# Performance work log

Hardware: AMD Instinct MI355X
Metric: run time of the kernel (lower is better)

The kernel has to match this reference:

```python
import jax, jax.numpy as jnp
import numpy as np

EMBED = 1024
HEADS = 16
HEAD_DIM = EMBED // HEADS


def setup_inputs() -> dict:
    key = jax.random.key(0)
    ks = jax.random.split(key, 5)
    scale = 1.0 / np.sqrt(EMBED)
    x = jax.random.normal(ks[0], (2, 2048, EMBED), dtype=jnp.float32)
    W_qkv = jax.random.normal(ks[1], (EMBED, 3 * EMBED), dtype=jnp.float32) * scale
    b_qkv = jnp.zeros((3 * EMBED,), dtype=jnp.float32)
    W_out = jax.random.normal(ks[2], (EMBED, EMBED), dtype=jnp.float32) * scale
    b_out = jnp.zeros((EMBED,), dtype=jnp.float32)
    return {"x": x, "W_qkv": W_qkv, "b_qkv": b_qkv, "W_out": W_out, "b_out": b_out}


def reference(x, W_qkv, b_qkv, W_out, b_out):
    B, S, E = x.shape
    # fused QKV projection
    qkv = x @ W_qkv + b_qkv                       # [B, S, 3E]
    qkv = qkv.reshape(B, S, HEADS, 3 * HEAD_DIM)
    q, k, v = jnp.split(qkv, 3, axis=-1)          # each [B, S, H, D]
    scale = jnp.sqrt(jnp.asarray(HEAD_DIM, dtype=x.dtype))
    # scores [B, H, S, S]
    scores = jnp.einsum('bqhd,bkhd->bhqk', q, k) / scale
    attn = jax.nn.softmax(scores, axis=-1)
    out = jnp.einsum('bhqk,bkhd->bqhd', attn, v).reshape(B, S, E)
    return out @ W_out + b_out
```

## Files before the change

kernel.cpp:

```cpp
#include <hip/hip_runtime.h>

#define B_    2
#define S_    2048
#define E_    1024
#define H_    16
#define D_    64
#define M_    4096
#define NQKV  3072
#define K_    1024

typedef __bf16 bf16;
typedef __attribute__((ext_vector_type(4))) __bf16 bf16x4;
typedef __attribute__((ext_vector_type(8))) __bf16 bf16x8;
typedef __attribute__((ext_vector_type(4))) float  f32x4;
typedef __attribute__((ext_vector_type(16))) float f32x16;

#define QSCALE 0.18033688f

__device__ __forceinline__ void gload_lds16(const void* g, void* l) {
    __builtin_amdgcn_global_load_lds(
        (const __attribute__((address_space(1))) void*)g,
        (__attribute__((address_space(3))) void*)l, 16, 0, 0);
}

__global__ __launch_bounds__(256) void cast_f32_bf16(
    const float* __restrict__ in, bf16* __restrict__ out, int n)
{
    int i = (blockIdx.x * 256 + threadIdx.x) * 4;
    if (i >= n) return;
    float4 v = *reinterpret_cast<const float4*>(in + i);
    bf16x4 o = { (bf16)v.x, (bf16)v.y, (bf16)v.z, (bf16)v.w };
    *reinterpret_cast<bf16x4*>(out + i) = o;
}

__global__ __launch_bounds__(256) void transpose_cast(
    const float* __restrict__ W, bf16* __restrict__ WT, int Krows, int Ncols)
{
    __shared__ bf16 tile[32][33];
    int bj = blockIdx.x;
    int bi = blockIdx.y;
    int tx = threadIdx.x & 31;
    int ty = threadIdx.x >> 5;
#pragma unroll
    for (int it = 0; it < 4; ++it) {
        int r = ty + it * 8;
        tile[r][tx] = (bf16)W[(size_t)(bi * 32 + r) * Ncols + bj * 32 + tx];
    }
    __syncthreads();
#pragma unroll
    for (int it = 0; it < 4; ++it) {
        int r = ty + it * 8;
        WT[(size_t)(bj * 32 + r) * Krows + bi * 32 + tx] = tile[tx][r];
    }
}

__device__ __forceinline__ void gemm_tile_128(
    const bf16* __restrict__ A, const bf16* __restrict__ BT, int K,
    int bm0, int bn0, f32x4 acc[4][4])
{
    __shared__ bf16 sA[128 * 32];
    __shared__ bf16 sB[128 * 32];
    const int tid  = threadIdx.x;
    const int lane = tid & 63;
    const int wave = tid >> 6;
    const int g    = lane >> 4;
    const int r    = lane & 15;
    const int wr   = wave >> 1, wc = wave & 1;
    const int lrow = lane >> 2;
    const int lcol = (lane & 3) * 8;

#pragma unroll
    for (int m = 0; m < 4; ++m)
#pragma unroll
        for (int n = 0; n < 4; ++n) acc[m][n] = (f32x4){0.f, 0.f, 0.f, 0.f};

    for (int k0 = 0; k0 < K; k0 += 32) {
#pragma unroll
        for (int j = 0; j < 2; ++j) {
            int r0 = wave * 32 + j * 16;
            gload_lds16(A  + (size_t)(bm0 + r0 + lrow) * K + k0 + lcol, &sA[r0 * 32]);
            gload_lds16(BT + (size_t)(bn0 + r0 + lrow) * K + k0 + lcol, &sB[r0 * 32]);
        }
        __syncthreads();
        bf16x8 af[4], bfr[4];
#pragma unroll
        for (int m = 0; m < 4; ++m)
            af[m] = *reinterpret_cast<const bf16x8*>(&sA[(wr * 64 + m * 16 + r) * 32 + g * 8]);
#pragma unroll
        for (int n = 0; n < 4; ++n)
            bfr[n] = *reinterpret_cast<const bf16x8*>(&sB[(wc * 64 + n * 16 + r) * 32 + g * 8]);
        __builtin_amdgcn_s_setprio(1);
#pragma unroll
        for (int m = 0; m < 4; ++m)
#pragma unroll
            for (int n = 0; n < 4; ++n)
                acc[m][n] = __builtin_amdgcn_mfma_f32_16x16x32_bf16(af[m], bfr[n], acc[m][n], 0, 0, 0);
        __builtin_amdgcn_s_setprio(0);
        __syncthreads();
    }
}

__global__ __launch_bounds__(256) void gemm_qkv(
    const bf16* __restrict__ xb, const bf16* __restrict__ WT,
    const float* __restrict__ bias,
    bf16* __restrict__ Qb, bf16* __restrict__ Kb, bf16* __restrict__ Vt)
{
    f32x4 acc[4][4];
    int bm0 = blockIdx.y * 128, bn0 = blockIdx.x * 128;
    gemm_tile_128(xb, WT, K_, bm0, bn0, acc);

    const int lane = threadIdx.x & 63, wave = threadIdx.x >> 6;
    const int g = lane >> 4, c = lane & 15;
    const int wr = wave >> 1, wc = wave & 1;
#pragma unroll
    for (int m = 0; m < 4; ++m) {
        int ibase = bm0 + wr * 64 + m * 16 + 4 * g;
        int b = ibase >> 11, s = ibase & 2047;
#pragma unroll
        for (int n = 0; n < 4; ++n) {
            int j = bn0 + wc * 64 + n * 16 + c;
            int h = j / 192, w = j % 192;
            int t = w >> 6, d = w & 63;
            float bj = bias[j];
            if (t == 2) {
                bf16x4 v4 = { (bf16)(acc[m][n][0] + bj), (bf16)(acc[m][n][1] + bj),
                              (bf16)(acc[m][n][2] + bj), (bf16)(acc[m][n][3] + bj) };
                *reinterpret_cast<bf16x4*>(
                    &Vt[((size_t)((b * H_ + h) * D_ + d)) * S_ + s]) = v4;
            } else {
                bf16* dst = (t == 0) ? Qb : Kb;
                float scale = (t == 0) ? QSCALE : 1.0f;
#pragma unroll
                for (int jj = 0; jj < 4; ++jj) {
                    size_t idx = ((size_t)((b * H_ + h) * S_ + s + jj)) * D_ + d;
                    dst[idx] = (bf16)((acc[m][n][jj] + bj) * scale);
                }
            }
        }
    }
}

__global__ __launch_bounds__(512, 4) void attn_kernel(
    const bf16* __restrict__ Qb, const bf16* __restrict__ Kb,
    const bf16* __restrict__ Vt, bf16* __restrict__ Ob)
{
    __shared__ __align__(16) char smem[37888];

    const int bh  = blockIdx.y;
    const int q0  = blockIdx.x * 128;
    const int tid = threadIdx.x, lane = tid & 63;
    const int qw   = (tid >> 6) & 3;
    const int half = tid >> 8;
    const int gtid = tid & 255;
    const int c = lane & 31;
    const int h = lane >> 5;

    bf16* sKh = reinterpret_cast<bf16*>(smem) + half * (64 * 72);
    bf16* sVh = reinterpret_cast<bf16*>(smem + 18432) + half * (64 * 72);
    float* mrg = reinterpret_cast<float*>(smem);
    float* ml  = reinterpret_cast<float*>(smem + 36864);

    const bf16* Qp = Qb + (size_t)bh * S_ * D_;
    const bf16* Kp = Kb + (size_t)bh * S_ * D_ + (size_t)half * 1024 * D_;
    const bf16* Vp = Vt + (size_t)bh * D_ * S_ + half * 1024;

    const int qrow = q0 + qw * 32 + c;
    bf16x8 qf[4];
#pragma unroll
    for (int kk = 0; kk < 4; ++kk)
        qf[kk] = *reinterpret_cast<const bf16x8*>(Qp + (size_t)qrow * D_ + kk * 16 + 8 * h);

    f32x16 acc[2];
#pragma unroll
    for (int t = 0; t < 2; ++t) acc[t] = (f32x16)(0.f);
    float m_run = -1e30f, l_run = 0.f;

    const int srow = gtid >> 3, sgi = gtid & 7;

    for (int kv0 = 0; kv0 < 1024; kv0 += 64) {
        __syncthreads();
#pragma unroll
        for (int i = 0; i < 2; ++i) {
            int row = srow + i * 32;
            *reinterpret_cast<uint4*>(&sKh[row * 72 + sgi * 8]) =
                *reinterpret_cast<const uint4*>(Kp + (size_t)(kv0 + row) * D_ + sgi * 8);
            *reinterpret_cast<uint4*>(&sVh[row * 72 + sgi * 8]) =
                *reinterpret_cast<const uint4*>(Vp + (size_t)row * S_ + kv0 + sgi * 8);
        }
        __syncthreads();

#pragma unroll
        for (int ks = 0; ks < 2; ++ks) {
            f32x16 sc = (f32x16)(0.f);
            __builtin_amdgcn_s_setprio(1);
#pragma unroll
            for (int kk = 0; kk < 4; ++kk) {
                bf16x8 kf = *reinterpret_cast<const bf16x8*>(
                    &sKh[(ks * 32 + c) * 72 + kk * 16 + 8 * h]);
                sc = __builtin_amdgcn_mfma_f32_32x32x16_bf16(kf, qf[kk], sc, 0, 0, 0);
            }
            __builtin_amdgcn_s_setprio(0);

            float t0 = fmaxf(fmaxf(sc[0], sc[1]), sc[2]);
            float t1 = fmaxf(fmaxf(sc[3], sc[4]), sc[5]);
            float t2 = fmaxf(fmaxf(sc[6], sc[7]), sc[8]);
            float t3 = fmaxf(fmaxf(sc[9], sc[10]), sc[11]);
            float t4 = fmaxf(fmaxf(sc[12], sc[13]), sc[14]);
            float t5 = fmaxf(fmaxf(t0, t1), sc[15]);
            float t6 = fmaxf(fmaxf(t2, t3), t4);
            float vmax = fmaxf(t5, t6);
            vmax = fmaxf(vmax, __shfl_xor(vmax, 32));
            if (__any(vmax > m_run + 8.0f)) {
                float mnew = fmaxf(m_run, vmax);
                float f = exp2f(m_run - mnew);
                l_run *= f;
#pragma unroll
                for (int t = 0; t < 2; ++t) acc[t] *= f;
                m_run = mnew;
            }
            float p[16];
            float ls = 0.f;
#pragma unroll
            for (int r = 0; r < 16; ++r) { p[r] = exp2f(sc[r] - m_run); ls += p[r]; }
            l_run += ls;

            unsigned w[8];
#pragma unroll
            for (int b = 0; b < 4; ++b) {
                union { bf16 x; unsigned short u; } a0, a1, a2, a3;
                a0.x = (bf16)p[4 * b + 0]; a1.x = (bf16)p[4 * b + 1];
                a2.x = (bf16)p[4 * b + 2]; a3.x = (bf16)p[4 * b + 3];
                w[2 * b]     = (unsigned)a0.u | ((unsigned)a1.u << 16);
                w[2 * b + 1] = (unsigned)a2.u | ((unsigned)a3.u << 16);
            }

#pragma unroll
            for (int kk = 0; kk < 2; ++kk) {
                unsigned s_lo = h ? w[4 * kk]     : w[4 * kk + 2];
                unsigned s_hi = h ? w[4 * kk + 1] : w[4 * kk + 3];
                unsigned r_lo = __shfl_xor(s_lo, 32);
                unsigned r_hi = __shfl_xor(s_hi, 32);
                union { bf16x8 v; unsigned u[4]; } pf;
                if (h == 0) {
                    pf.u[0] = w[4 * kk]; pf.u[1] = w[4 * kk + 1];
                    pf.u[2] = r_lo;      pf.u[3] = r_hi;
                } else {
                    pf.u[0] = r_lo;      pf.u[1] = r_hi;
                    pf.u[2] = w[4 * kk + 2]; pf.u[3] = w[4 * kk + 3];
                }
                __builtin_amdgcn_s_setprio(1);
#pragma unroll
                for (int t = 0; t < 2; ++t) {
                    bf16x8 vf = *reinterpret_cast<const bf16x8*>(
                        &sVh[(32 * t + c) * 72 + ks * 32 + kk * 16 + 8 * h]);
                    acc[t] = __builtin_amdgcn_mfma_f32_32x32x16_bf16(vf, pf.v, acc[t], 0, 0, 0);
                }
                __builtin_amdgcn_s_setprio(0);
            }
        }
    }

    float l_tot = l_run + __shfl_xor(l_run, 32);

    __syncthreads();
    if (half == 1) {
        float4* dst = reinterpret_cast<float4*>(&mrg[(qw * 64 + lane) * 33]);
#pragma unroll
        for (int t = 0; t < 2; ++t)
#pragma unroll
            for (int v = 0; v < 4; ++v)
                dst[t * 4 + v] = make_float4(acc[t][4 * v + 0], acc[t][4 * v + 1],
                                             acc[t][4 * v + 2], acc[t][4 * v + 3]);
        if (lane < 32) { ml[(qw * 32 + lane) * 2 + 0] = m_run;
                         ml[(qw * 32 + lane) * 2 + 1] = l_tot; }
    }
    __syncthreads();

    if (half == 0) {
        float m1 = ml[(qw * 32 + c) * 2 + 0], l1 = ml[(qw * 32 + c) * 2 + 1];
        float mm = fmaxf(m_run, m1);
        float f0 = exp2f(m_run - mm), f1 = exp2f(m1 - mm);
        float li = 1.0f / (l_tot * f0 + l1 * f1);
        float g0 = f0 * li, g1 = f1 * li;
        const float4* src = reinterpret_cast<const float4*>(&mrg[(qw * 64 + lane) * 33]);
        float o[2][16];
#pragma unroll
        for (int t = 0; t < 2; ++t)
#pragma unroll
            for (int v = 0; v < 4; ++v) {
                float4 a1 = src[t * 4 + v];
                o[t][4 * v + 0] = acc[t][4 * v + 0] * g0 + a1.x * g1;
                o[t][4 * v + 1] = acc[t][4 * v + 1] * g0 + a1.y * g1;
                o[t][4 * v + 2] = acc[t][4 * v + 2] * g0 + a1.z * g1;
                o[t][4 * v + 3] = acc[t][4 * v + 3] * g0 + a1.w * g1;
            }

        bf16* so = reinterpret_cast<bf16*>(&mrg[(size_t)qw * 64 * 33]);
#pragma unroll
        for (int t = 0; t < 2; ++t)
#pragma unroll
            for (int b = 0; b < 4; ++b) {
                bf16x4 v4 = { (bf16)o[t][4 * b + 0], (bf16)o[t][4 * b + 1],
                              (bf16)o[t][4 * b + 2], (bf16)o[t][4 * b + 3] };
                *reinterpret_cast<bf16x4*>(&so[c * 72 + t * 32 + b * 8 + 4 * h]) = v4;
            }
        const int bb = bh >> 4, hh = bh & 15;
#pragma unroll
        for (int i = 0; i < 4; ++i) {
            int chunk = lane + 64 * i;
            int row = chunk >> 3, gi = chunk & 7;
            uint4 val = *reinterpret_cast<uint4*>(&so[row * 72 + gi * 8]);
            *reinterpret_cast<uint4*>(
                Ob + ((size_t)(bb * S_ + q0 + qw * 32 + row)) * E_ + hh * 64 + gi * 8) = val;
        }
    }
}

__global__ __launch_bounds__(256) void gemm_out(
    const bf16* __restrict__ Ob, const bf16* __restrict__ WT,
    const float* __restrict__ bias, float* __restrict__ out)
{
    f32x4 acc[4][4];
    int bm0 = blockIdx.y * 128, bn0 = blockIdx.x * 128;
    gemm_tile_128(Ob, WT, K_, bm0, bn0, acc);

    const int lane = threadIdx.x & 63, wave = threadIdx.x >> 6;
    const int g = lane >> 4, c = lane & 15;
    const int wr = wave >> 1, wc = wave & 1;
#pragma unroll
    for (int m = 0; m < 4; ++m) {
        int ibase = bm0 + wr * 64 + m * 16 + 4 * g;
#pragma unroll
        for (int n = 0; n < 4; ++n) {
            int j = bn0 + wc * 64 + n * 16 + c;
            float bj = bias[j];
#pragma unroll
            for (int jj = 0; jj < 4; ++jj) {
                int row = ibase + jj;
                out[(size_t)row * E_ + j] = acc[m][n][jj] + bj;
            }
        }
    }
}

extern "C" void kernel_launch(void* const* d_in, const int* in_sizes, int n_in,
                              void* d_out, int out_size, void* d_ws, size_t ws_size,
                              hipStream_t stream)
{
    const float* x     = (const float*)d_in[0];
    const float* W_qkv = (const float*)d_in[1];
    const float* b_qkv = (const float*)d_in[2];
    const float* W_out = (const float*)d_in[3];
    const float* b_out = (const float*)d_in[4];
    float* out = (float*)d_out;

    char* ws = (char*)d_ws;
    bf16* xb    = (bf16*)(ws);
    bf16* WqkvT = (bf16*)(ws + (8u  << 20));
    bf16* WoutT = (bf16*)(ws + (14u << 20));
    bf16* Qb    = (bf16*)(ws + (16u << 20));
    bf16* Kb    = (bf16*)(ws + (24u << 20));
    bf16* Vt    = (bf16*)(ws + (32u << 20));
    bf16* Ob    = (bf16*)(ws + (40u << 20));

    cast_f32_bf16<<<4096, 256, 0, stream>>>(x, xb, M_ * K_);
    transpose_cast<<<dim3(NQKV / 32, K_ / 32), 256, 0, stream>>>(W_qkv, WqkvT, K_, NQKV);
    transpose_cast<<<dim3(E_ / 32, K_ / 32), 256, 0, stream>>>(W_out, WoutT, K_, E_);
    gemm_qkv<<<dim3(NQKV / 128, M_ / 128), 256, 0, stream>>>(xb, WqkvT, b_qkv, Qb, Kb, Vt);
    attn_kernel<<<dim3(S_ / 128, B_ * H_), 512, 0, stream>>>(Qb, Kb, Vt, Ob);
    gemm_out<<<dim3(E_ / 128, M_ / 128), 256, 0, stream>>>(Ob, WoutT, b_out, out);
}
```

Measured before the change: 148.3 us.

## Split attention KV range four ways with 64-row query tiles and swizzled blocks

The attention kernel now gives each block 64 query rows instead of 128 and splits the KV sequence four ways across 8 waves (2 query waves x 4 KV quarters). It processes 32-key tiles and merges the partial softmax states in a two-level LDS reduction. The grid doubles to 1024 blocks, and block IDs are swizzled so consecutive blocks spread across heads. This aims to raise parallelism and occupancy, but it re-reads K and V for every 64 query rows instead of every 128, adds extra synchronizations in the merge, and uses smaller MFMA tiles per barrier.

```diff
diff --git a/kernel.cpp b/kernel.cpp
--- a/kernel.cpp
+++ b/kernel.cpp
@@ -144,25 +144,28 @@
     const bf16* __restrict__ Qb, const bf16* __restrict__ Kb,
     const bf16* __restrict__ Vt, bf16* __restrict__ Ob)
 {
-    __shared__ __align__(16) char smem[37888];
-
-    const int bh  = blockIdx.y;
-    const int q0  = blockIdx.x * 128;
+    __shared__ __align__(16) char smem[40960];
+
+    const int bid = blockIdx.y * 32 + blockIdx.x;
+    const int swz = (bid & 7) * 128 + (bid >> 3);
+    const int bh   = swz >> 5;
+    const int q0   = (swz & 31) * 64;
+
     const int tid = threadIdx.x, lane = tid & 63;
-    const int qw   = (tid >> 6) & 3;
-    const int half = tid >> 8;
-    const int gtid = tid & 255;
+    const int w  = tid >> 6;
+    const int qw = w & 1, kq = w >> 1;
+    const int gtid = tid & 127;
     const int c = lane & 31;
     const int h = lane >> 5;
 
-    bf16* sKh = reinterpret_cast<bf16*>(smem) + half * (64 * 72);
-    bf16* sVh = reinterpret_cast<bf16*>(smem + 18432) + half * (64 * 72);
+    bf16*  sK  = reinterpret_cast<bf16*>(smem) + kq * (32 * 72);
+    bf16*  sV  = reinterpret_cast<bf16*>(smem + 18432) + kq * (64 * 40);
     float* mrg = reinterpret_cast<float*>(smem);
-    float* ml  = reinterpret_cast<float*>(smem + 36864);
+    float* ml  = reinterpret_cast<float*>(smem + 38912);
 
     const bf16* Qp = Qb + (size_t)bh * S_ * D_;
-    const bf16* Kp = Kb + (size_t)bh * S_ * D_ + (size_t)half * 1024 * D_;
-    const bf16* Vp = Vt + (size_t)bh * D_ * S_ + half * 1024;
+    const bf16* Kp = Kb + (size_t)bh * S_ * D_ + (size_t)kq * 512 * D_;
+    const bf16* Vp = Vt + (size_t)bh * D_ * S_ + kq * 512;
 
     const int qrow = q0 + qw * 32 + c;
     bf16x8 qf[4];
@@ -175,127 +178,161 @@
     for (int t = 0; t < 2; ++t) acc[t] = (f32x16)(0.f);
     float m_run = -1e30f, l_run = 0.f;
 
-    const int srow = gtid >> 3, sgi = gtid & 7;
-
-    for (int kv0 = 0; kv0 < 1024; kv0 += 64) {
+    for (int kv0 = 0; kv0 < 512; kv0 += 32) {
         __syncthreads();
 #pragma unroll
         for (int i = 0; i < 2; ++i) {
-            int row = srow + i * 32;
-            *reinterpret_cast<uint4*>(&sKh[row * 72 + sgi * 8]) =
-                *reinterpret_cast<const uint4*>(Kp + (size_t)(kv0 + row) * D_ + sgi * 8);
-            *reinterpret_cast<uint4*>(&sVh[row * 72 + sgi * 8]) =
-                *reinterpret_cast<const uint4*>(Vp + (size_t)row * S_ + kv0 + sgi * 8);
+            int ch = gtid + i * 128;
+            int rK = ch >> 3, cK = (ch & 7) * 8;
+            *reinterpret_cast<uint4*>(&sK[rK * 72 + cK]) =
+                *reinterpret_cast<const uint4*>(Kp + (size_t)(kv0 + rK) * D_ + cK);
+            int rV = ch >> 2, cV = (ch & 3) * 8;
+            *reinterpret_cast<uint4*>(&sV[rV * 40 + cV]) =
+                *reinterpret_cast<const uint4*>(Vp + (size_t)rV * S_ + kv0 + cV);
         }
         __syncthreads();
 
-#pragma unroll
-        for (int ks = 0; ks < 2; ++ks) {
-            f32x16 sc = (f32x16)(0.f);
+        f32x16 sc = (f32x16)(0.f);
+        __builtin_amdgcn_s_setprio(1);
+#pragma unroll
+        for (int kk = 0; kk < 4; ++kk) {
+            bf16x8 kf = *reinterpret_cast<const bf16x8*>(&sK[c * 72 + kk * 16 + 8 * h]);
+            sc = __builtin_amdgcn_mfma_f32_32x32x16_bf16(kf, qf[kk], sc, 0, 0, 0);
+        }
+        __builtin_amdgcn_s_setprio(0);
+
+        float t0 = fmaxf(fmaxf(sc[0], sc[1]), sc[2]);
+        float t1 = fmaxf(fmaxf(sc[3], sc[4]), sc[5]);
+        float t2 = fmaxf(fmaxf(sc[6], sc[7]), sc[8]);
+        float t3 = fmaxf(fmaxf(sc[9], sc[10]), sc[11]);
+        float t4 = fmaxf(fmaxf(sc[12], sc[13]), sc[14]);
+        float t5 = fmaxf(fmaxf(t0, t1), sc[15]);
+        float t6 = fmaxf(fmaxf(t2, t3), t4);
+        float vmax = fmaxf(t5, t6);
+        vmax = fmaxf(vmax, __shfl_xor(vmax, 32));
+        if (__any(vmax > m_run + 8.0f)) {
+            float mnew = fmaxf(m_run, vmax);
+            float f = exp2f(m_run - mnew);
+            l_run *= f;
+#pragma unroll
+            for (int t = 0; t < 2; ++t) acc[t] *= f;
+            m_run = mnew;
+        }
+        float p[16];
+        float ls = 0.f;
+#pragma unroll
+        for (int r = 0; r < 16; ++r) { p[r] = exp2f(sc[r] - m_run); ls += p[r]; }
+        l_run += ls;
+
+        unsigned wv[8];
+#pragma unroll
+        for (int b = 0; b < 4; ++b) {
+            union { bf16 x; unsigned short u; } a0, a1, a2, a3;
+            a0.x = (bf16)p[4 * b + 0]; a1.x = (bf16)p[4 * b + 1];
+            a2.x = (bf16)p[4 * b + 2]; a3.x = (bf16)p[4 * b + 3];
+            wv[2 * b]     = (unsigned)a0.u | ((unsigned)a1.u << 16);
+            wv[2 * b + 1] = (unsigned)a2.u | ((unsigned)a3.u << 16);
+        }
+
+#pragma unroll
+        for (int kk = 0; kk < 2; ++kk) {
+            unsigned s_lo = h ? wv[4 * kk]     : wv[4 * kk + 2];
+            unsigned s_hi = h ? wv[4 * kk + 1] : wv[4 * kk + 3];
+            unsigned r_lo = __shfl_xor(s_lo, 32);
+            unsigned r_hi = __shfl_xor(s_hi, 32);
+            union { bf16x8 v; unsigned u[4]; } pf;
+            if (h == 0) {
+                pf.u[0] = wv[4 * kk]; pf.u[1] = wv[4 * kk + 1];
+                pf.u[2] = r_lo;       pf.u[3] = r_hi;
+            } else {
+                pf.u[0] = r_lo;       pf.u[1] = r_hi;
+                pf.u[2] = wv[4 * kk + 2]; pf.u[3] = wv[4 * kk + 3];
+            }
             __builtin_amdgcn_s_setprio(1);
 #pragma unroll
-            for (int kk = 0; kk < 4; ++kk) {
-                bf16x8 kf = *reinterpret_cast<const bf16x8*>(
-                    &sKh[(ks * 32 + c) * 72 + kk * 16 + 8 * h]);
-                sc = __builtin_amdgcn_mfma_f32_32x32x16_bf16(kf, qf[kk], sc, 0, 0, 0);
+            for (int t = 0; t < 2; ++t) {
+                bf16x8 vf = *reinterpret_cast<const bf16x8*>(
+                    &sV[(32 * t + c) * 40 + kk * 16 + 8 * h]);
+                acc[t] = __builtin_amdgcn_mfma_f32_32x32x16_bf16(vf, pf.v, acc[t], 0, 0, 0);
             }
             __builtin_amdgcn_s_setprio(0);
-
-            float t0 = fmaxf(fmaxf(sc[0], sc[1]), sc[2]);
-            float t1 = fmaxf(fmaxf(sc[3], sc[4]), sc[5]);
-            float t2 = fmaxf(fmaxf(sc[6], sc[7]), sc[8]);
-            float t3 = fmaxf(fmaxf(sc[9], sc[10]), sc[11]);
-            float t4 = fmaxf(fmaxf(sc[12], sc[13]), sc[14]);
-            float t5 = fmaxf(fmaxf(t0, t1), sc[15]);
-            float t6 = fmaxf(fmaxf(t2, t3), t4);
-            float vmax = fmaxf(t5, t6);
-            vmax = fmaxf(vmax, __shfl_xor(vmax, 32));
-            if (__any(vmax > m_run + 8.0f)) {
-                float mnew = fmaxf(m_run, vmax);
-                float f = exp2f(m_run - mnew);
-                l_run *= f;
-#pragma unroll
-                for (int t = 0; t < 2; ++t) acc[t] *= f;
-                m_run = mnew;
-            }
-            float p[16];
-            float ls = 0.f;
-#pragma unroll
-            for (int r = 0; r < 16; ++r) { p[r] = exp2f(sc[r] - m_run); ls += p[r]; }
-            l_run += ls;
-
-            unsigned w[8];
-#pragma unroll
-            for (int b = 0; b < 4; ++b) {
-                union { bf16 x; unsigned short u; } a0, a1, a2, a3;
-                a0.x = (bf16)p[4 * b + 0]; a1.x = (bf16)p[4 * b + 1];
-                a2.x = (bf16)p[4 * b + 2]; a3.x = (bf16)p[4 * b + 3];
-                w[2 * b]     = (unsigned)a0.u | ((unsigned)a1.u << 16);
-                w[2 * b + 1] = (unsigned)a2.u | ((unsigned)a3.u << 16);
-            }
-
-#pragma unroll
-            for (int kk = 0; kk < 2; ++kk) {
-                unsigned s_lo = h ? w[4 * kk]     : w[4 * kk + 2];
-                unsigned s_hi = h ? w[4 * kk + 1] : w[4 * kk + 3];
-                unsigned r_lo = __shfl_xor(s_lo, 32);
-                unsigned r_hi = __shfl_xor(s_hi, 32);
-                union { bf16x8 v; unsigned u[4]; } pf;
-                if (h == 0) {
-                    pf.u[0] = w[4 * kk]; pf.u[1] = w[4 * kk + 1];
-                    pf.u[2] = r_lo;      pf.u[3] = r_hi;
-                } else {
-                    pf.u[0] = r_lo;      pf.u[1] = r_hi;
-                    pf.u[2] = w[4 * kk + 2]; pf.u[3] = w[4 * kk + 3];
-                }
-                __builtin_amdgcn_s_setprio(1);
-#pragma unroll
-                for (int t = 0; t < 2; ++t) {
-                    bf16x8 vf = *reinterpret_cast<const bf16x8*>(
-                        &sVh[(32 * t + c) * 72 + ks * 32 + kk * 16 + 8 * h]);
-                    acc[t] = __builtin_amdgcn_mfma_f32_32x32x16_bf16(vf, pf.v, acc[t], 0, 0, 0);
-                }
-                __builtin_amdgcn_s_setprio(0);
-            }
         }
     }
 
     float l_tot = l_run + __shfl_xor(l_run, 32);
 
     __syncthreads();
-    if (half == 1) {
-        float4* dst = reinterpret_cast<float4*>(&mrg[(qw * 64 + lane) * 33]);
+    if (kq >= 2) {
+        float* dst = &mrg[((qw * 2 + (kq - 2)) * 64 + lane) * 36];
 #pragma unroll
         for (int t = 0; t < 2; ++t)
 #pragma unroll
             for (int v = 0; v < 4; ++v)
-                dst[t * 4 + v] = make_float4(acc[t][4 * v + 0], acc[t][4 * v + 1],
-                                             acc[t][4 * v + 2], acc[t][4 * v + 3]);
-        if (lane < 32) { ml[(qw * 32 + lane) * 2 + 0] = m_run;
-                         ml[(qw * 32 + lane) * 2 + 1] = l_tot; }
+                reinterpret_cast<float4*>(dst)[t * 4 + v] =
+                    make_float4(acc[t][4 * v + 0], acc[t][4 * v + 1],
+                                acc[t][4 * v + 2], acc[t][4 * v + 3]);
+        if (lane < 32) {
+            ml[((qw * 4 + kq) * 32 + c) * 2 + 0] = m_run;
+            ml[((qw * 4 + kq) * 32 + c) * 2 + 1] = l_tot;
+        }
     }
     __syncthreads();
-
-    if (half == 0) {
-        float m1 = ml[(qw * 32 + c) * 2 + 0], l1 = ml[(qw * 32 + c) * 2 + 1];
+    if (kq < 2) {
+        const float* src = &mrg[((qw * 2 + kq) * 64 + lane) * 36];
+        float m1 = ml[((qw * 4 + kq + 2) * 32 + c) * 2 + 0];
+        float l1 = ml[((qw * 4 + kq + 2) * 32 + c) * 2 + 1];
+        float mm = fmaxf(m_run, m1);
+        float f0 = exp2f(m_run - mm), f1 = exp2f(m1 - mm);
+#pragma unroll
+        for (int t = 0; t < 2; ++t)
+#pragma unroll
+            for (int v = 0; v < 4; ++v) {
+                float4 a1 = reinterpret_cast<const float4*>(src)[t * 4 + v];
+                acc[t][4 * v + 0] = acc[t][4 * v + 0] * f0 + a1.x * f1;
+                acc[t][4 * v + 1] = acc[t][4 * v + 1] * f0 + a1.y * f1;
+                acc[t][4 * v + 2] = acc[t][4 * v + 2] * f0 + a1.z * f1;
+                acc[t][4 * v + 3] = acc[t][4 * v + 3] * f0 + a1.w * f1;
+            }
+        l_tot = l_tot * f0 + l1 * f1;
+        m_run = mm;
+    }
+    __syncthreads();
+    if (kq == 1) {
+        float* dst = &mrg[((qw * 2 + 0) * 64 + lane) * 36];
+#pragma unroll
+        for (int t = 0; t < 2; ++t)
+#pragma unroll
+            for (int v = 0; v < 4; ++v)
+                reinterpret_cast<float4*>(dst)[t * 4 + v] =
+                    make_float4(acc[t][4 * v + 0], acc[t][4 * v + 1],
+                                acc[t][4 * v + 2], acc[t][4 * v + 3]);
+        if (lane < 32) {
+            ml[((qw * 4 + 1) * 32 + c) * 2 + 0] = m_run;
+            ml[((qw * 4 + 1) * 32 + c) * 2 + 1] = l_tot;
+        }
+    }
+    __syncthreads();
+    if (kq == 0) {
+        const float* src = &mrg[((qw * 2 + 0) * 64 + lane) * 36];
+        float m1 = ml[((qw * 4 + 1) * 32 + c) * 2 + 0];
+        float l1 = ml[((qw * 4 + 1) * 32 + c) * 2 + 1];
         float mm = fmaxf(m_run, m1);
         float f0 = exp2f(m_run - mm), f1 = exp2f(m1 - mm);
         float li = 1.0f / (l_tot * f0 + l1 * f1);
         float g0 = f0 * li, g1 = f1 * li;
-        const float4* src = reinterpret_cast<const float4*>(&mrg[(qw * 64 + lane) * 33]);
         float o[2][16];
 #pragma unroll
         for (int t = 0; t < 2; ++t)
 #pragma unroll
             for (int v = 0; v < 4; ++v) {
-                float4 a1 = src[t * 4 + v];
+                float4 a1 = reinterpret_cast<const float4*>(src)[t * 4 + v];
                 o[t][4 * v + 0] = acc[t][4 * v + 0] * g0 + a1.x * g1;
                 o[t][4 * v + 1] = acc[t][4 * v + 1] * g0 + a1.y * g1;
                 o[t][4 * v + 2] = acc[t][4 * v + 2] * g0 + a1.z * g1;
                 o[t][4 * v + 3] = acc[t][4 * v + 3] * g0 + a1.w * g1;
             }
 
-        bf16* so = reinterpret_cast<bf16*>(&mrg[(size_t)qw * 64 * 33]);
+        bf16* so = reinterpret_cast<bf16*>(&mrg[(qw * 2 + 1) * 64 * 36]);
 #pragma unroll
         for (int t = 0; t < 2; ++t)
 #pragma unroll
@@ -367,6 +404,6 @@
     transpose_cast<<<dim3(NQKV / 32, K_ / 32), 256, 0, stream>>>(W_qkv, WqkvT, K_, NQKV);
     transpose_cast<<<dim3(E_ / 32, K_ / 32), 256, 0, stream>>>(W_out, WoutT, K_, E_);
     gemm_qkv<<<dim3(NQKV / 128, M_ / 128), 256, 0, stream>>>(xb, WqkvT, b_qkv, Qb, Kb, Vt);
-    attn_kernel<<<dim3(S_ / 128, B_ * H_), 512, 0, stream>>>(Qb, Kb, Vt, Ob);
+    attn_kernel<<<dim3(S_ / 64, B_ * H_), 512, 0, stream>>>(Qb, Kb, Vt, Ob);
     gemm_out<<<dim3(E_ / 128, M_ / 128), 256, 0, stream>>>(Ob, WoutT, b_out, out);
 }
```

Result: slower. 160.7 us (+8.4%).

## Double-buffer K/V tiles in attention via register prefetch and swizzle block order

Applied to the files above, without the earlier changes.

The attention kernel now prefetches the next K/V tile into registers while computing on the current LDS buffer, then writes it to the alternate LDS buffer, removing one barrier per iteration and overlapping global loads with MFMA work. It also remaps block indices so consecutive blocks spread across heads, which may improve cache and channel locality. LDS use doubles to about 74KB, which limits occupancy to fewer blocks per CU, and register pressure rises from the held prefetch data.

```diff
diff --git a/kernel.cpp b/kernel.cpp
--- a/kernel.cpp
+++ b/kernel.cpp
@@ -144,10 +144,13 @@
     const bf16* __restrict__ Qb, const bf16* __restrict__ Kb,
     const bf16* __restrict__ Vt, bf16* __restrict__ Ob)
 {
-    __shared__ __align__(16) char smem[37888];
-
-    const int bh  = blockIdx.y;
-    const int q0  = blockIdx.x * 128;
+    __shared__ __align__(16) char smem[75776];
+
+    const int bid = blockIdx.y * 16 + blockIdx.x;
+    const int swz = (bid & 7) * 64 + (bid >> 3);
+    const int bh  = swz >> 4;
+    const int q0  = (swz & 15) * 128;
+
     const int tid = threadIdx.x, lane = tid & 63;
     const int qw   = (tid >> 6) & 3;
     const int half = tid >> 8;
@@ -155,10 +158,10 @@
     const int c = lane & 31;
     const int h = lane >> 5;
 
-    bf16* sKh = reinterpret_cast<bf16*>(smem) + half * (64 * 72);
-    bf16* sVh = reinterpret_cast<bf16*>(smem + 18432) + half * (64 * 72);
     float* mrg = reinterpret_cast<float*>(smem);
-    float* ml  = reinterpret_cast<float*>(smem + 36864);
+    float* ml  = reinterpret_cast<float*>(smem + 73728);
+#define KBASE(hf, cb) (reinterpret_cast<bf16*>(smem) + ((hf) * 2 + (cb)) * (64 * 72))
+#define VBASE(hf, cb) (reinterpret_cast<bf16*>(smem + 36864) + ((hf) * 2 + (cb)) * (64 * 72))
 
     const bf16* Qp = Qb + (size_t)bh * S_ * D_;
     const bf16* Kp = Kb + (size_t)bh * S_ * D_ + (size_t)half * 1024 * D_;
@@ -176,18 +179,39 @@
     float m_run = -1e30f, l_run = 0.f;
 
     const int srow = gtid >> 3, sgi = gtid & 7;
-
+    uint4 rk[2], rv[2];
+
+#pragma unroll
+    for (int i = 0; i < 2; ++i) {
+        int row = srow + i * 32;
+        rk[i] = *reinterpret_cast<const uint4*>(Kp + (size_t)row * D_ + sgi * 8);
+        rv[i] = *reinterpret_cast<const uint4*>(Vp + (size_t)row * S_ + sgi * 8);
+    }
+    {
+        bf16* sKw = KBASE(half, 0);
+        bf16* sVw = VBASE(half, 0);
+#pragma unroll
+        for (int i = 0; i < 2; ++i) {
+            int row = srow + i * 32;
+            *reinterpret_cast<uint4*>(&sKw[row * 72 + sgi * 8]) = rk[i];
+            *reinterpret_cast<uint4*>(&sVw[row * 72 + sgi * 8]) = rv[i];
+        }
+    }
+
+    int cur = 0;
     for (int kv0 = 0; kv0 < 1024; kv0 += 64) {
         __syncthreads();
-#pragma unroll
-        for (int i = 0; i < 2; ++i) {
-            int row = srow + i * 32;
-            *reinterpret_cast<uint4*>(&sKh[row * 72 + sgi * 8]) =
-                *reinterpret_cast<const uint4*>(Kp + (size_t)(kv0 + row) * D_ + sgi * 8);
-            *reinterpret_cast<uint4*>(&sVh[row * 72 + sgi * 8]) =
-                *reinterpret_cast<const uint4*>(Vp + (size_t)row * S_ + kv0 + sgi * 8);
-        }
-        __syncthreads();
+        const bool more = (kv0 + 64) < 1024;
+        if (more) {
+#pragma unroll
+            for (int i = 0; i < 2; ++i) {
+                int row = srow + i * 32;
+                rk[i] = *reinterpret_cast<const uint4*>(Kp + (size_t)(kv0 + 64 + row) * D_ + sgi * 8);
+                rv[i] = *reinterpret_cast<const uint4*>(Vp + (size_t)row * S_ + kv0 + 64 + sgi * 8);
+            }
+        }
+        const bf16* sKh = KBASE(half, cur);
+        const bf16* sVh = VBASE(half, cur);
 
 #pragma unroll
         for (int ks = 0; ks < 2; ++ks) {
@@ -258,6 +282,18 @@
                 __builtin_amdgcn_s_setprio(0);
             }
         }
+
+        if (more) {
+            bf16* sKw = KBASE(half, cur ^ 1);
+            bf16* sVw = VBASE(half, cur ^ 1);
+#pragma unroll
+            for (int i = 0; i < 2; ++i) {
+                int row = srow + i * 32;
+                *reinterpret_cast<uint4*>(&sKw[row * 72 + sgi * 8]) = rk[i];
+                *reinterpret_cast<uint4*>(&sVw[row * 72 + sgi * 8]) = rv[i];
+            }
+        }
+        cur ^= 1;
     }
 
     float l_tot = l_run + __shfl_xor(l_run, 32);
@@ -314,6 +350,8 @@
                 Ob + ((size_t)(bb * S_ + q0 + qw * 32 + row)) * E_ + hh * 64 + gi * 8) = val;
         }
     }
+#undef KBASE
+#undef VBASE
 }
 
 __global__ __launch_bounds__(256) void gemm_out(
```

Result: slower. 167.6 us (+13.0%).
